# Performance work log

Hardware: AMD Instinct MI355X
Metric: run time of the kernel (lower is better)

The kernel has to match this reference:

```python
import jax, jax.numpy as jnp
import numpy as np

DIM = 512
HEADS = 8
DIM_HEAD = 64
HIDDEN = HEADS * DIM_HEAD  # 512


def setup_inputs() -> dict:
    key = jax.random.key(0)
    k1, k2, k3, k4 = jax.random.split(key, 4)
    x = jax.random.normal(k1, (8, DIM, 64, 64), dtype=jnp.float32)
    # 1x1 conv weights stored as [out_ch, in_ch] (kernel spatial dims are 1)
    w_qkv = jax.random.normal(k2, (HIDDEN * 3, DIM), dtype=jnp.float32) * (1.0 / np.sqrt(DIM))
    w_out = jax.random.normal(k3, (DIM, HIDDEN), dtype=jnp.float32) * (1.0 / np.sqrt(HIDDEN))
    b_out = jax.random.normal(k4, (DIM,), dtype=jnp.float32) * 0.01
    return {"x": x, "w_qkv": w_qkv, "w_out": w_out, "b_out": b_out}


def reference(x, w_qkv, w_out, b_out):
    b, c, h, w = x.shape
    n = h * w
    # to_qkv: 1x1 conv == per-pixel GEMM over channels
    qkv = jnp.einsum('bchw,oc->bohw', x, w_qkv)            # [b, 3*hidden, h, w]
    qkv = qkv.reshape(b, 3, HEADS, DIM_HEAD, n)            # matches torch reshape order
    q, k, v = qkv[:, 0], qkv[:, 1], qkv[:, 2]              # each [b, heads, dim_head, n]
    k = jax.nn.softmax(k, axis=-1)                          # softmax over spatial positions
    context = jnp.einsum('bhdn,bhen->bhde', k, v)          # [b, heads, d, e] kv outer-product
    out = jnp.einsum('bhde,bhdn->bhen', context, q)        # query readout [b, heads, e, n]
    out = out.reshape(b, HEADS * DIM_HEAD, h, w)
    # to_out: 1x1 conv with bias
    return jnp.einsum('bchw,oc->bohw', out, w_out) + b_out[None, :, None, None]
```

## Files before the change

### kernel.cpp

```cpp
#include <hip/hip_runtime.h>
#include <hip/hip_bf16.h>
#include <math.h>

#define NB    8
#define CDIM  512
#define NSP   4096
#define NHEAD 8

typedef short short8 __attribute__((ext_vector_type(8)));
typedef float f32x4  __attribute__((ext_vector_type(4)));

__device__ __forceinline__ unsigned short f2bf(float f) {
    unsigned int u = __float_as_uint(f);
    u += 0x7fff + ((u >> 16) & 1);
    return (unsigned short)(u >> 16);
}
__device__ __forceinline__ float bf2f(unsigned short s) {
    return __uint_as_float(((unsigned int)s) << 16);
}
__device__ __forceinline__ void gld_lds16(const void* g, void* s) {
    __builtin_amdgcn_global_load_lds(
        (const __attribute__((address_space(1))) unsigned int*)g,
        (__attribute__((address_space(3))) unsigned int*)s, 16, 0, 0);
}
__device__ __forceinline__ void split8(const float* s, short8& hi, short8& lo) {
    float4 a = *reinterpret_cast<const float4*>(s);
    float4 b = *reinterpret_cast<const float4*>(s + 4);
    float v[8] = {a.x, a.y, a.z, a.w, b.x, b.y, b.z, b.w};
    #pragma unroll
    for (int j = 0; j < 8; ++j) {
        unsigned short hh = f2bf(v[j]);
        hi[j] = (short)hh;
        lo[j] = (short)f2bf(v[j] - bf2f(hh));
    }
}

__global__ __launch_bounds__(256) void convert_x(const float* __restrict__ x,
    unsigned short* __restrict__ xh, unsigned short* __restrict__ xl)
{
    const int cb4 = blockIdx.x;
    const int kt  = blockIdx.y;
    const int b   = blockIdx.z;
    const int tid = threadIdx.x;

    __shared__ float sx[32][65];

    const int r  = tid >> 3;
    const int c8 = (tid & 7) * 8;
    const float* xp = x + ((long)b * CDIM + kt * 32 + r) * NSP + cb4 * 64 + c8;
    float4 v0 = *reinterpret_cast<const float4*>(xp);
    float4 v1 = *reinterpret_cast<const float4*>(xp + 4);
    sx[r][c8 + 0] = v0.x; sx[r][c8 + 1] = v0.y; sx[r][c8 + 2] = v0.z; sx[r][c8 + 3] = v0.w;
    sx[r][c8 + 4] = v1.x; sx[r][c8 + 5] = v1.y; sx[r][c8 + 6] = v1.z; sx[r][c8 + 7] = v1.w;
    __syncthreads();

    const int cb_l  = tid >> 6;
    const int lane  = tid & 63;
    const int cb    = cb4 * 4 + cb_l;
    const int col_l = cb_l * 16 + (lane & 15);
    const int k0    = (lane >> 4) * 8;
    short8 hv, lv;
    #pragma unroll
    for (int j = 0; j < 8; ++j) {
        float v = sx[k0 + j][col_l];
        unsigned short hh = f2bf(v);
        hv[j] = (short)hh;
        lv[j] = (short)f2bf(v - bf2f(hh));
    }
    const long base = (((long)(b * 256 + cb) * 16 + kt) * 512) + lane * 8;
    *reinterpret_cast<short8*>(xh + base) = hv;
    *reinterpret_cast<short8*>(xl + base) = lv;
}

__global__ __launch_bounds__(64) void convert_w(const float* __restrict__ w,
    unsigned short* __restrict__ wh, unsigned short* __restrict__ wl)
{
    const int lane = threadIdx.x & 63;
    const int rb = blockIdx.x;
    const int kt = blockIdx.y;
    const int row = rb * 16 + (lane & 15);
    const int k0  = kt * 32 + (lane >> 4) * 8;
    const float* wp = w + (long)row * CDIM + k0;
    const long base = ((long)rb * 16 + kt) * 512 + lane * 8;
    short8 hv, lv;
    #pragma unroll
    for (int j = 0; j < 8; ++j) {
        float v = wp[j];
        unsigned short h = f2bf(v);
        hv[j] = (short)h;
        lv[j] = (short)f2bf(v - bf2f(h));
    }
    *reinterpret_cast<short8*>(wh + base) = hv;
    *reinterpret_cast<short8*>(wl + base) = lv;
}

__global__ __launch_bounds__(64) void convert_b(const float* __restrict__ src,
    int ld, unsigned short* __restrict__ bh, unsigned short* __restrict__ bl)
{
    const int lane = threadIdx.x & 63;
    const int cb = blockIdx.x;
    const int kt = blockIdx.y;
    const int col = cb * 16 + (lane & 15);
    const int k0  = kt * 32 + (lane >> 4) * 8;
    const float* sp = src + (long)k0 * ld + col;
    const long base = ((long)cb * 16 + kt) * 512 + lane * 8;
    short8 hv, lv;
    #pragma unroll
    for (int j = 0; j < 8; ++j) {
        float v = sp[(long)j * ld];
        unsigned short h = f2bf(v);
        hv[j] = (short)h;
        lv[j] = (short)f2bf(v - bf2f(h));
    }
    *reinterpret_cast<short8*>(bh + base) = hv;
    *reinterpret_cast<short8*>(bl + base) = lv;
}

__global__ __launch_bounds__(256, 2) void fused_kv_ctx(
    const unsigned short* __restrict__ Ah, const unsigned short* __restrict__ Al,
    const unsigned short* __restrict__ Bh, const unsigned short* __restrict__ Bl,
    float* __restrict__ ctx, float* __restrict__ ssum)
{
    const int ch = blockIdx.x;
    const int h  = blockIdx.y;
    const int b  = blockIdx.z;
    const int tid  = threadIdx.x;
    const int lane = tid & 63;
    const int wid  = tid >> 6;
    const int wr = wid >> 1, wc = wid & 1;

    __shared__ __align__(16) char lds[49152];

    f32x4 acc[4][8];
    #pragma unroll
    for (int m = 0; m < 4; ++m)
        #pragma unroll
        for (int n = 0; n < 8; ++n)
            acc[m][n] = (f32x4){0.f, 0.f, 0.f, 0.f};

    const unsigned short* srcs[12];
    #pragma unroll
    for (int i = 0; i < 12; ++i) {
        const int blk = wid * 12 + i;
        const unsigned short* s;
        if (blk < 16) {
            const int sub = blk & 7;
            const int rb = (sub < 4) ? (h * 4 + sub) : (32 + h * 4 + (sub - 4));
            s = ((blk < 8) ? Ah : Al) + ((long)(rb * 16) << 9);
        } else {
            const int j = (blk - 16) & 15;
            const int cb = ch * 16 + j;
            s = ((blk < 32) ? Bh : Bl) + (((long)(b * 256 + cb) * 16) << 9);
        }
        srcs[i] = s + lane * 8;
    }

    for (int kt = 0; kt < 16; ++kt) {
        #pragma unroll
        for (int i = 0; i < 12; ++i) {
            gld_lds16(srcs[i], lds + (wid * 12 + i) * 1024);
            srcs[i] += 512;
        }
        __syncthreads();

        short8 ah[4], al[4];
        #pragma unroll
        for (int m = 0; m < 4; ++m) {
            ah[m] = *reinterpret_cast<const short8*>(lds +        (wr * 4 + m) * 1024 + lane * 16);
            al[m] = *reinterpret_cast<const short8*>(lds + 8192 + (wr * 4 + m) * 1024 + lane * 16);
        }
        #pragma unroll
        for (int n = 0; n < 8; ++n) {
            short8 bh = *reinterpret_cast<const short8*>(lds + 16384 + (wc * 8 + n) * 1024 + lane * 16);
            short8 bl = *reinterpret_cast<const short8*>(lds + 32768 + (wc * 8 + n) * 1024 + lane * 16);
            #pragma unroll
            for (int m = 0; m < 4; ++m) {
                acc[m][n] = __builtin_amdgcn_mfma_f32_16x16x32_bf16(ah[m], bh, acc[m][n], 0, 0, 0);
                acc[m][n] = __builtin_amdgcn_mfma_f32_16x16x32_bf16(ah[m], bl, acc[m][n], 0, 0, 0);
                acc[m][n] = __builtin_amdgcn_mfma_f32_16x16x32_bf16(al[m], bh, acc[m][n], 0, 0, 0);
            }
        }
        __syncthreads();
    }

    if (wr == 0) {
        #pragma unroll
        for (int m = 0; m < 4; ++m)
            #pragma unroll
            for (int j = 0; j < 4; ++j) {
                float s = 0.f;
                #pragma unroll
                for (int n = 0; n < 8; ++n) {
                    float e = __expf(acc[m][n][j]);
                    acc[m][n][j] = e;
                    s += e;
                }
                s += __shfl_xor(s, 1); s += __shfl_xor(s, 2);
                s += __shfl_xor(s, 4); s += __shfl_xor(s, 8);
                if ((lane & 15) == 0)
                    atomicAdd(&ssum[b * 512 + h * 64 + m * 16 + (lane >> 4) * 4 + j], s);
            }
    }

    float* Plds = (float*)lds;
    float* Vlds = (float*)(lds + 64 * 68 * 4);
    f32x4 acc2[2][2];
    #pragma unroll
    for (int mi = 0; mi < 2; ++mi)
        #pragma unroll
        for (int ni = 0; ni < 2; ++ni) acc2[mi][ni] = (f32x4){0.f, 0.f, 0.f, 0.f};

    #pragma unroll
    for (int q = 0; q < 4; ++q) {
        __syncthreads();
        if (wc == (q >> 1)) {
            float* T = (wr == 0) ? Plds : Vlds;
            #pragma unroll
            for (int m = 0; m < 4; ++m)
                #pragma unroll
                for (int nn = 0; nn < 4; ++nn)
                    #pragma unroll
                    for (int j = 0; j < 4; ++j)
                        T[(m * 16 + (lane >> 4) * 4 + j) * 68 + nn * 16 + (lane & 15)]
                            = acc[m][(q & 1) * 4 + nn][j];
        }
        __syncthreads();

        #pragma unroll
        for (int ks = 0; ks < 2; ++ks) {
            const int kcol = ks * 32 + (lane >> 4) * 8;
            short8 pa_h[2], pa_l[2], vb_h[2], vb_l[2];
            #pragma unroll
            for (int mi = 0; mi < 2; ++mi)
                split8(&Plds[((wr * 2 + mi) * 16 + (lane & 15)) * 68 + kcol], pa_h[mi], pa_l[mi]);
            #pragma unroll
            for (int ni = 0; ni < 2; ++ni)
                split8(&Vlds[((wc * 2 + ni) * 16 + (lane & 15)) * 68 + kcol], vb_h[ni], vb_l[ni]);
            #pragma unroll
            for (int mi = 0; mi < 2; ++mi)
                #pragma unroll
                for (int ni = 0; ni < 2; ++ni) {
                    acc2[mi][ni] = __builtin_amdgcn_mfma_f32_16x16x32_bf16(pa_h[mi], vb_h[ni], acc2[mi][ni], 0, 0, 0);
                    acc2[mi][ni] = __builtin_amdgcn_mfma_f32_16x16x32_bf16(pa_h[mi], vb_l[ni], acc2[mi][ni], 0, 0, 0);
                    acc2[mi][ni] = __builtin_amdgcn_mfma_f32_16x16x32_bf16(pa_l[mi], vb_h[ni], acc2[mi][ni], 0, 0, 0);
                }
        }
    }

    float* cp = ctx + (long)(b * NHEAD + h) * 4096;
    #pragma unroll
    for (int mi = 0; mi < 2; ++mi)
        #pragma unroll
        for (int ni = 0; ni < 2; ++ni) {
            const int d0 = (wr * 2 + mi) * 16;
            const int e0 = (wc * 2 + ni) * 16;
            #pragma unroll
            for (int j = 0; j < 4; ++j)
                atomicAdd(&cp[(d0 + (lane >> 4) * 4 + j) * 64 + e0 + (lane & 15)], acc2[mi][ni][j]);
        }
}

template<int NKT, bool BIAS>
__global__ __launch_bounds__(512, 2) void gemm_mfma256(
    const unsigned short* __restrict__ Ah, const unsigned short* __restrict__ Al,
    const unsigned short* __restrict__ Bh, const unsigned short* __restrict__ Bl,
    float* __restrict__ C, const float* __restrict__ bias,
    int N, int aBatchRB, int bBatchCB, long cBatch)
{
    const int b    = blockIdx.z;
    const int tid  = threadIdx.x;
    const int lane = tid & 63;
    const int wid  = tid >> 6;
    const int wr   = wid >> 2;
    const int wc   = wid & 3;

    __shared__ __align__(16) char lds[2][65536];

    f32x4 acc[8][4];
    #pragma unroll
    for (int m = 0; m < 8; ++m)
        #pragma unroll
        for (int n = 0; n < 4; ++n)
            acc[m][n] = (f32x4){0.f, 0.f, 0.f, 0.f};

    const int rb0 = b * aBatchRB + blockIdx.y * 16;
    const int cb0 = b * bBatchCB + blockIdx.x * 16;

    const unsigned short* srcs[8];
    #pragma unroll
    for (int i = 0; i < 8; ++i) {
        const int blk = wid * 8 + i;
        const int sub = blk & 15;
        const unsigned short* s;
        if (blk < 16)      s = Ah + ((long)(rb0 + sub) * NKT << 9);
        else if (blk < 32) s = Al + ((long)(rb0 + sub) * NKT << 9);
        else if (blk < 48) s = Bh + ((long)(cb0 + sub) * NKT << 9);
        else               s = Bl + ((long)(cb0 + sub) * NKT << 9);
        srcs[i] = s + lane * 8;
    }
    const int ldsoff = wid * 8192;

    #pragma unroll
    for (int i = 0; i < 8; ++i) {
        gld_lds16(srcs[i], &lds[0][ldsoff + i * 1024]);
        srcs[i] += 512;
    }

    int cur = 0;
    for (int kt = 0; kt < NKT; ++kt) {
        if (kt + 1 < NKT) {
            #pragma unroll
            for (int i = 0; i < 8; ++i) {
                gld_lds16(srcs[i], &lds[cur ^ 1][ldsoff + i * 1024]);
                srcs[i] += 512;
            }
            asm volatile("s_waitcnt vmcnt(8)" ::: "memory");
        } else {
            asm volatile("s_waitcnt vmcnt(0)" ::: "memory");
        }
        __builtin_amdgcn_s_barrier();

        const char* L = lds[cur];
        short8 ah[8], al[8];
        #pragma unroll
        for (int m = 0; m < 8; ++m) {
            ah[m] = *reinterpret_cast<const short8*>(L +         (wr * 8 + m) * 1024 + lane * 16);
            al[m] = *reinterpret_cast<const short8*>(L + 16384 + (wr * 8 + m) * 1024 + lane * 16);
        }
        __builtin_amdgcn_s_setprio(1);
        #pragma unroll
        for (int n = 0; n < 4; ++n) {
            short8 bh = *reinterpret_cast<const short8*>(L + 32768 + (wc * 4 + n) * 1024 + lane * 16);
            short8 bl = *reinterpret_cast<const short8*>(L + 49152 + (wc * 4 + n) * 1024 + lane * 16);
            #pragma unroll
            for (int m = 0; m < 8; ++m) {
                acc[m][n] = __builtin_amdgcn_mfma_f32_16x16x32_bf16(ah[m], bh, acc[m][n], 0, 0, 0);
                acc[m][n] = __builtin_amdgcn_mfma_f32_16x16x32_bf16(ah[m], bl, acc[m][n], 0, 0, 0);
                acc[m][n] = __builtin_amdgcn_mfma_f32_16x16x32_bf16(al[m], bh, acc[m][n], 0, 0, 0);
            }
        }
        __builtin_amdgcn_s_setprio(0);
        asm volatile("" ::: "memory");
        __builtin_amdgcn_s_barrier();
        asm volatile("" ::: "memory");
        cur ^= 1;
    }

    const int row0 = blockIdx.y * 256 + wr * 128;
    const int col0 = blockIdx.x * 256 + wc * 64;
    float* Cb = C + (long)b * cBatch;
    #pragma unroll
    for (int m = 0; m < 8; ++m)
        #pragma unroll
        for (int n = 0; n < 4; ++n) {
            const int col = col0 + n * 16 + (lane & 15);
            #pragma unroll
            for (int j = 0; j < 4; ++j) {
                const int row = row0 + m * 16 + (lane >> 4) * 4 + j;
                float v = acc[m][n][j];
                if (BIAS) v += bias[row];
                Cb[(long)row * N + col] = v;
            }
        }
}

template<int NKT, bool BIAS>
__global__ __launch_bounds__(256) void gemm_mfma(
    const unsigned short* __restrict__ Ah, const unsigned short* __restrict__ Al,
    const unsigned short* __restrict__ Bh, const unsigned short* __restrict__ Bl,
    float* __restrict__ C, const float* __restrict__ bias,
    int N, int aBatchRB, int bBatchCB, long cBatch)
{
    const int b    = blockIdx.z;
    const int tid  = threadIdx.x;
    const int lane = tid & 63;
    const int wid  = tid >> 6;
    const int wr   = wid >> 1;
    const int wc   = wid & 1;

    __shared__ __align__(16) char lds[32768];

    f32x4 acc[4][4];
    #pragma unroll
    for (int m = 0; m < 4; ++m)
        #pragma unroll
        for (int n = 0; n < 4; ++n) acc[m][n] = (f32x4){0.f, 0.f, 0.f, 0.f};

    const int rb0 = b * aBatchRB + blockIdx.y * 8;
    const int cb0 = b * bBatchCB + blockIdx.x * 8;

    const unsigned short* srcs[8];
    #pragma unroll
    for (int i = 0; i < 8; ++i) {
        const int blk = wid * 8 + i;
        const int sub = blk & 7;
        const unsigned short* s;
        if (blk < 8)       s = Ah + ((long)(rb0 + sub) * NKT << 9);
        else if (blk < 16) s = Al + ((long)(rb0 + sub) * NKT << 9);
        else if (blk < 24) s = Bh + ((long)(cb0 + sub) * NKT << 9);
        else               s = Bl + ((long)(cb0 + sub) * NKT << 9);
        srcs[i] = s + lane * 8;
    }

    for (int kt = 0; kt < NKT; ++kt) {
        #pragma unroll
        for (int i = 0; i < 8; ++i) {
            gld_lds16(srcs[i], lds + (wid * 8 + i) * 1024);
            srcs[i] += 512;
        }
        __syncthreads();

        short8 ah[4], al[4], bh[4], bl[4];
        #pragma unroll
        for (int m = 0; m < 4; ++m) {
            ah[m] = *reinterpret_cast<const short8*>(lds +         (wr * 4 + m) * 1024 + lane * 16);
            al[m] = *reinterpret_cast<const short8*>(lds +  8192 + (wr * 4 + m) * 1024 + lane * 16);
        }
        #pragma unroll
        for (int n = 0; n < 4; ++n) {
            bh[n] = *reinterpret_cast<const short8*>(lds + 16384 + (wc * 4 + n) * 1024 + lane * 16);
            bl[n] = *reinterpret_cast<const short8*>(lds + 24576 + (wc * 4 + n) * 1024 + lane * 16);
        }
        #pragma unroll
        for (int m = 0; m < 4; ++m)
            #pragma unroll
            for (int n = 0; n < 4; ++n) {
                acc[m][n] = __builtin_amdgcn_mfma_f32_16x16x32_bf16(ah[m], bh[n], acc[m][n], 0, 0, 0);
                acc[m][n] = __builtin_amdgcn_mfma_f32_16x16x32_bf16(ah[m], bl[n], acc[m][n], 0, 0, 0);
                acc[m][n] = __builtin_amdgcn_mfma_f32_16x16x32_bf16(al[m], bh[n], acc[m][n], 0, 0, 0);
            }
        __syncthreads();
    }

    const int row0 = blockIdx.y * 128 + wr * 64;
    const int col0 = blockIdx.x * 128 + wc * 64;
    float* Cb = C + (long)b * cBatch;
    #pragma unroll
    for (int m = 0; m < 4; ++m)
        #pragma unroll
        for (int n = 0; n < 4; ++n) {
            const int col = col0 + n * 16 + (lane & 15);
            #pragma unroll
            for (int j = 0; j < 4; ++j) {
                const int row = row0 + m * 16 + (lane >> 4) * 4 + j;
                float v = acc[m][n][j];
                if (BIAS) v += bias[row];
                Cb[(long)row * N + col] = v;
            }
        }
}

__global__ __launch_bounds__(256) void zero_buf(float* p, int n) {
    for (int i = blockIdx.x * 256 + threadIdx.x; i < n; i += gridDim.x * 256) p[i] = 0.f;
}

__global__ __launch_bounds__(256) void ctx_fold2(
    const float* __restrict__ w_out, const float* __restrict__ ctx,
    const float* __restrict__ ssum,
    unsigned short* __restrict__ amh, unsigned short* __restrict__ aml)
{
    const int o0 = blockIdx.x * 64;
    const int h  = blockIdx.y;
    const int b  = blockIdx.z;
    const int tid = threadIdx.x;

    __shared__ float Wo[64][65];
    __shared__ float Ct[64][65];
    __shared__ float At[64][65];

    for (int idx = tid; idx < 64 * 16; idx += 256) {
        const int r = idx >> 4;
        const int c = (idx & 15) * 4;
        float4 w4 = *reinterpret_cast<const float4*>(&w_out[(long)(o0 + r) * CDIM + h * 64 + c]);
        Wo[r][c + 0] = w4.x; Wo[r][c + 1] = w4.y; Wo[r][c + 2] = w4.z; Wo[r][c + 3] = w4.w;
        float4 c4 = *reinterpret_cast<const float4*>(&ctx[(((long)(b * NHEAD + h) * 64 + r) * 64) + c]);
        Ct[r][c + 0] = c4.x; Ct[r][c + 1] = c4.y; Ct[r][c + 2] = c4.z; Ct[r][c + 3] = c4.w;
    }
    __syncthreads();

    const int to = tid >> 4, td = tid & 15;
    float acc[4][4];
    #pragma unroll
    for (int i = 0; i < 4; ++i)
        #pragma unroll
        for (int j = 0; j < 4; ++j) acc[i][j] = 0.f;

    for (int e = 0; e < 64; ++e) {
        float ro[4], rd[4];
        #pragma unroll
        for (int i = 0; i < 4; ++i) ro[i] = Wo[to * 4 + i][e];
        #pragma unroll
        for (int j = 0; j < 4; ++j) rd[j] = Ct[td * 4 + j][e];
        #pragma unroll
        for (int i = 0; i < 4; ++i)
            #pragma unroll
            for (int j = 0; j < 4; ++j) acc[i][j] += ro[i] * rd[j];
    }

    #pragma unroll
    for (int j = 0; j < 4; ++j) {
        const float s = 1.f / ssum[b * 512 + h * 64 + td * 4 + j];
        #pragma unroll
        for (int i = 0; i < 4; ++i)
            At[to * 4 + i][td * 4 + j] = acc[i][j] * s;
    }
    __syncthreads();

    const int g = tid >> 6, lane = tid & 63;
    #pragma unroll
    for (int kt_l = 0; kt_l < 2; ++kt_l) {
        short8 hv, lv;
        #pragma unroll
        for (int jj = 0; jj < 8; ++jj) {
            float v = At[g * 16 + (lane & 15)][kt_l * 32 + (lane >> 4) * 8 + jj];
            unsigned short hh = f2bf(v);
            hv[jj] = (short)hh;
            lv[jj] = (short)f2bf(v - bf2f(hh));
        }
        const long base = (((long)(b * 32 + (o0 >> 4) + g) * 16) + (h * 2 + kt_l)) * 512 + lane * 8;
        *reinterpret_cast<short8*>(amh + base) = hv;
        *reinterpret_cast<short8*>(aml + base) = lv;
    }
}

extern "C" void kernel_launch(void* const* d_in, const int* in_sizes, int n_in,
                              void* d_out, int out_size, void* d_ws, size_t ws_size,
                              hipStream_t stream) {
    (void)in_sizes; (void)n_in; (void)out_size; (void)ws_size;
    const float* x     = (const float*)d_in[0];
    const float* w_qkv = (const float*)d_in[1];
    const float* w_out = (const float*)d_in[2];
    const float* b_out = (const float*)d_in[3];
    float* out = (float*)d_out;

    char* ws = (char*)d_ws;
    unsigned short* xh   = (unsigned short*)(ws + 134217728L);
    unsigned short* xl   = (unsigned short*)(ws + 167772160L);
    unsigned short* wkvh = (unsigned short*)(ws + 201326592L);
    unsigned short* wkvl = (unsigned short*)(ws + 202375168L);
    float*          ssum = (float*)(ws + 203423744L);
    float*          ctx  = (float*)(ws + 203440128L);
    float*          W3   = (float*)(ws + 8388608L);
    unsigned short* amh  = (unsigned short*)(ws + 16777216L);
    unsigned short* aml  = (unsigned short*)(ws + 20971520L);
    unsigned short* wqh  = (unsigned short*)(ws + 25165824L);
    unsigned short* wql  = (unsigned short*)(ws + 26214400L);
    unsigned short* w3h  = (unsigned short*)(ws + 27262976L);
    unsigned short* w3l  = (unsigned short*)(ws + 31457280L);

    convert_x<<<dim3(64, 16, NB), 256, 0, stream>>>(x, xh, xl);
    convert_w<<<dim3(64, 16), 64, 0, stream>>>(w_qkv + 512L * CDIM, wkvh, wkvl);
    zero_buf<<<256, 256, 0, stream>>>(ssum, (16384 + 1048576) / 4);

    fused_kv_ctx<<<dim3(16, NHEAD, NB), 256, 0, stream>>>(
        wkvh, wkvl, xh, xl, ctx, ssum);

    convert_b<<<dim3(32, 16), 64, 0, stream>>>(w_qkv, CDIM, wqh, wql);

    ctx_fold2<<<dim3(8, NHEAD, NB), 256, 0, stream>>>(w_out, ctx, ssum, amh, aml);

    gemm_mfma<16, false><<<dim3(4, 4, NB), 256, 0, stream>>>(
        amh, aml, wqh, wql, W3, nullptr, CDIM, 32, 0, (long)CDIM * CDIM);

    convert_w<<<dim3(256, 16), 64, 0, stream>>>(W3, w3h, w3l);
    gemm_mfma256<16, true><<<dim3(16, 2, NB), 512, 0, stream>>>(
        w3h, w3l, xh, xl, out, b_out, NSP, 32, 256, (long)CDIM * NSP);
}
```

Measured before the change: 219.1 us.

## Widen fused_kv_ctx to 512 threads and fuse W3 GEMM with bf16 split conversion

The fused K/V context kernel now runs 8 waves per block instead of 4. Each wave handles half as many column tiles, which cuts accumulator registers and allows more waves to be resident. Separately, the W3 GEMM epilogue now stages its results through LDS and writes the bf16 hi/lo split tiles directly. This removes the fp32 W3 round trip through global memory and one kernel launch. The cost is extra LDS staging and more barriers in the epilogue.

```diff
diff --git a/kernel.cpp b/kernel.cpp
--- a/kernel.cpp
+++ b/kernel.cpp
@@ -116,7 +116,7 @@
     *reinterpret_cast<short8*>(bl + base) = lv;
 }
 
-__global__ __launch_bounds__(256, 2) void fused_kv_ctx(
+__global__ __launch_bounds__(512, 4) void fused_kv_ctx(
     const unsigned short* __restrict__ Ah, const unsigned short* __restrict__ Al,
     const unsigned short* __restrict__ Bh, const unsigned short* __restrict__ Bl,
     float* __restrict__ ctx, float* __restrict__ ssum)
@@ -127,21 +127,22 @@
     const int tid  = threadIdx.x;
     const int lane = tid & 63;
     const int wid  = tid >> 6;
-    const int wr = wid >> 1, wc = wid & 1;
+    const int wr = wid >> 2;
+    const int wc = wid & 3;
 
     __shared__ __align__(16) char lds[49152];
 
-    f32x4 acc[4][8];
+    f32x4 acc[4][4];
     #pragma unroll
     for (int m = 0; m < 4; ++m)
         #pragma unroll
-        for (int n = 0; n < 8; ++n)
+        for (int n = 0; n < 4; ++n)
             acc[m][n] = (f32x4){0.f, 0.f, 0.f, 0.f};
 
-    const unsigned short* srcs[12];
-    #pragma unroll
-    for (int i = 0; i < 12; ++i) {
-        const int blk = wid * 12 + i;
+    const unsigned short* srcs[6];
+    #pragma unroll
+    for (int i = 0; i < 6; ++i) {
+        const int blk = wid * 6 + i;
         const unsigned short* s;
         if (blk < 16) {
             const int sub = blk & 7;
@@ -157,8 +158,8 @@
 
     for (int kt = 0; kt < 16; ++kt) {
         #pragma unroll
-        for (int i = 0; i < 12; ++i) {
-            gld_lds16(srcs[i], lds + (wid * 12 + i) * 1024);
+        for (int i = 0; i < 6; ++i) {
+            gld_lds16(srcs[i], lds + (wid * 6 + i) * 1024);
             srcs[i] += 512;
         }
         __syncthreads();
@@ -170,9 +171,9 @@
             al[m] = *reinterpret_cast<const short8*>(lds + 8192 + (wr * 4 + m) * 1024 + lane * 16);
         }
         #pragma unroll
-        for (int n = 0; n < 8; ++n) {
-            short8 bh = *reinterpret_cast<const short8*>(lds + 16384 + (wc * 8 + n) * 1024 + lane * 16);
-            short8 bl = *reinterpret_cast<const short8*>(lds + 32768 + (wc * 8 + n) * 1024 + lane * 16);
+        for (int n = 0; n < 4; ++n) {
+            short8 bh = *reinterpret_cast<const short8*>(lds + 16384 + (wc * 4 + n) * 1024 + lane * 16);
+            short8 bl = *reinterpret_cast<const short8*>(lds + 32768 + (wc * 4 + n) * 1024 + lane * 16);
             #pragma unroll
             for (int m = 0; m < 4; ++m) {
                 acc[m][n] = __builtin_amdgcn_mfma_f32_16x16x32_bf16(ah[m], bh, acc[m][n], 0, 0, 0);
@@ -190,7 +191,7 @@
             for (int j = 0; j < 4; ++j) {
                 float s = 0.f;
                 #pragma unroll
-                for (int n = 0; n < 8; ++n) {
+                for (int n = 0; n < 4; ++n) {
                     float e = __expf(acc[m][n][j]);
                     acc[m][n][j] = e;
                     s += e;
@@ -204,60 +205,52 @@
 
     float* Plds = (float*)lds;
     float* Vlds = (float*)(lds + 64 * 68 * 4);
-    f32x4 acc2[2][2];
-    #pragma unroll
-    for (int mi = 0; mi < 2; ++mi)
-        #pragma unroll
-        for (int ni = 0; ni < 2; ++ni) acc2[mi][ni] = (f32x4){0.f, 0.f, 0.f, 0.f};
+    f32x4 acc2[2];
+    acc2[0] = (f32x4){0.f, 0.f, 0.f, 0.f};
+    acc2[1] = (f32x4){0.f, 0.f, 0.f, 0.f};
 
     #pragma unroll
     for (int q = 0; q < 4; ++q) {
         __syncthreads();
-        if (wc == (q >> 1)) {
+        if (wc == q) {
             float* T = (wr == 0) ? Plds : Vlds;
             #pragma unroll
             for (int m = 0; m < 4; ++m)
                 #pragma unroll
-                for (int nn = 0; nn < 4; ++nn)
+                for (int n = 0; n < 4; ++n)
                     #pragma unroll
                     for (int j = 0; j < 4; ++j)
-                        T[(m * 16 + (lane >> 4) * 4 + j) * 68 + nn * 16 + (lane & 15)]
-                            = acc[m][(q & 1) * 4 + nn][j];
+                        T[(m * 16 + (lane >> 4) * 4 + j) * 68 + n * 16 + (lane & 15)]
+                            = acc[m][n][j];
         }
         __syncthreads();
 
         #pragma unroll
         for (int ks = 0; ks < 2; ++ks) {
             const int kcol = ks * 32 + (lane >> 4) * 8;
-            short8 pa_h[2], pa_l[2], vb_h[2], vb_l[2];
+            short8 pa_h[2], pa_l[2], vb_h, vb_l;
             #pragma unroll
             for (int mi = 0; mi < 2; ++mi)
-                split8(&Plds[((wr * 2 + mi) * 16 + (lane & 15)) * 68 + kcol], pa_h[mi], pa_l[mi]);
-            #pragma unroll
-            for (int ni = 0; ni < 2; ++ni)
-                split8(&Vlds[((wc * 2 + ni) * 16 + (lane & 15)) * 68 + kcol], vb_h[ni], vb_l[ni]);
-            #pragma unroll
-            for (int mi = 0; mi < 2; ++mi)
-                #pragma unroll
-                for (int ni = 0; ni < 2; ++ni) {
-                    acc2[mi][ni] = __builtin_amdgcn_mfma_f32_16x16x32_bf16(pa_h[mi], vb_h[ni], acc2[mi][ni], 0, 0, 0);
-                    acc2[mi][ni] = __builtin_amdgcn_mfma_f32_16x16x32_bf16(pa_h[mi], vb_l[ni], acc2[mi][ni], 0, 0, 0);
-                    acc2[mi][ni] = __builtin_amdgcn_mfma_f32_16x16x32_bf16(pa_l[mi], vb_h[ni], acc2[mi][ni], 0, 0, 0);
-                }
+                split8(&Plds[(wr * 32 + mi * 16 + (lane & 15)) * 68 + kcol], pa_h[mi], pa_l[mi]);
+            split8(&Vlds[(wc * 16 + (lane & 15)) * 68 + kcol], vb_h, vb_l);
+            #pragma unroll
+            for (int mi = 0; mi < 2; ++mi) {
+                acc2[mi] = __builtin_amdgcn_mfma_f32_16x16x32_bf16(pa_h[mi], vb_h, acc2[mi], 0, 0, 0);
+                acc2[mi] = __builtin_amdgcn_mfma_f32_16x16x32_bf16(pa_h[mi], vb_l, acc2[mi], 0, 0, 0);
+                acc2[mi] = __builtin_amdgcn_mfma_f32_16x16x32_bf16(pa_l[mi], vb_h, acc2[mi], 0, 0, 0);
+            }
         }
     }
 
     float* cp = ctx + (long)(b * NHEAD + h) * 4096;
     #pragma unroll
-    for (int mi = 0; mi < 2; ++mi)
-        #pragma unroll
-        for (int ni = 0; ni < 2; ++ni) {
-            const int d0 = (wr * 2 + mi) * 16;
-            const int e0 = (wc * 2 + ni) * 16;
-            #pragma unroll
-            for (int j = 0; j < 4; ++j)
-                atomicAdd(&cp[(d0 + (lane >> 4) * 4 + j) * 64 + e0 + (lane & 15)], acc2[mi][ni][j]);
-        }
+    for (int mi = 0; mi < 2; ++mi) {
+        const int d0 = wr * 32 + mi * 16;
+        const int e  = wc * 16 + (lane & 15);
+        #pragma unroll
+        for (int j = 0; j < 4; ++j)
+            atomicAdd(&cp[(d0 + (lane >> 4) * 4 + j) * 64 + e], acc2[mi][j]);
+    }
 }
 
 template<int NKT, bool BIAS>
@@ -364,12 +357,14 @@
         }
 }
 
-template<int NKT, bool BIAS>
-__global__ __launch_bounds__(256) void gemm_mfma(
+__global__ __launch_bounds__(256) void zero_buf(float* p, int n) {
+    for (int i = blockIdx.x * 256 + threadIdx.x; i < n; i += gridDim.x * 256) p[i] = 0.f;
+}
+
+__global__ __launch_bounds__(256) void gemm_w3(
     const unsigned short* __restrict__ Ah, const unsigned short* __restrict__ Al,
     const unsigned short* __restrict__ Bh, const unsigned short* __restrict__ Bl,
-    float* __restrict__ C, const float* __restrict__ bias,
-    int N, int aBatchRB, int bBatchCB, long cBatch)
+    unsigned short* __restrict__ w3h, unsigned short* __restrict__ w3l)
 {
     const int b    = blockIdx.z;
     const int tid  = threadIdx.x;
@@ -378,7 +373,7 @@
     const int wr   = wid >> 1;
     const int wc   = wid & 1;
 
-    __shared__ __align__(16) char lds[32768];
+    __shared__ __align__(16) char lds[64 * 132 * 4];
 
     f32x4 acc[4][4];
     #pragma unroll
@@ -386,8 +381,8 @@
         #pragma unroll
         for (int n = 0; n < 4; ++n) acc[m][n] = (f32x4){0.f, 0.f, 0.f, 0.f};
 
-    const int rb0 = b * aBatchRB + blockIdx.y * 8;
-    const int cb0 = b * bBatchCB + blockIdx.x * 8;
+    const int rb0 = b * 32 + blockIdx.y * 8;
+    const int cb0 = blockIdx.x * 8;
 
     const unsigned short* srcs[8];
     #pragma unroll
@@ -395,14 +390,14 @@
         const int blk = wid * 8 + i;
         const int sub = blk & 7;
         const unsigned short* s;
-        if (blk < 8)       s = Ah + ((long)(rb0 + sub) * NKT << 9);
-        else if (blk < 16) s = Al + ((long)(rb0 + sub) * NKT << 9);
-        else if (blk < 24) s = Bh + ((long)(cb0 + sub) * NKT << 9);
-        else               s = Bl + ((long)(cb0 + sub) * NKT << 9);
+        if (blk < 8)       s = Ah + ((long)(rb0 + sub) * 16 << 9);
+        else if (blk < 16) s = Al + ((long)(rb0 + sub) * 16 << 9);
+        else if (blk < 24) s = Bh + ((long)(cb0 + sub) * 16 << 9);
+        else               s = Bl + ((long)(cb0 + sub) * 16 << 9);
         srcs[i] = s + lane * 8;
     }
 
-    for (int kt = 0; kt < NKT; ++kt) {
+    for (int kt = 0; kt < 16; ++kt) {
         #pragma unroll
         for (int i = 0; i < 8; ++i) {
             gld_lds16(srcs[i], lds + (wid * 8 + i) * 1024);
@@ -432,26 +427,40 @@
         __syncthreads();
     }
 
-    const int row0 = blockIdx.y * 128 + wr * 64;
-    const int col0 = blockIdx.x * 128 + wc * 64;
-    float* Cb = C + (long)b * cBatch;
-    #pragma unroll
-    for (int m = 0; m < 4; ++m)
-        #pragma unroll
-        for (int n = 0; n < 4; ++n) {
-            const int col = col0 + n * 16 + (lane & 15);
-            #pragma unroll
-            for (int j = 0; j < 4; ++j) {
-                const int row = row0 + m * 16 + (lane >> 4) * 4 + j;
-                float v = acc[m][n][j];
-                if (BIAS) v += bias[row];
-                Cb[(long)row * N + col] = v;
-            }
-        }
-}
-
-__global__ __launch_bounds__(256) void zero_buf(float* p, int n) {
-    for (int i = blockIdx.x * 256 + threadIdx.x; i < n; i += gridDim.x * 256) p[i] = 0.f;
+    float* Ct = (float*)lds;
+    #pragma unroll
+    for (int hf = 0; hf < 2; ++hf) {
+        __syncthreads();
+        if (wr == hf) {
+            #pragma unroll
+            for (int m = 0; m < 4; ++m)
+                #pragma unroll
+                for (int n = 0; n < 4; ++n)
+                    #pragma unroll
+                    for (int j = 0; j < 4; ++j)
+                        Ct[(m * 16 + (lane >> 4) * 4 + j) * 132 + wc * 64 + n * 16 + (lane & 15)]
+                            = acc[m][n][j];
+        }
+        __syncthreads();
+        #pragma unroll
+        for (int i = 0; i < 4; ++i) {
+            const int blkid = wid * 4 + i;
+            const int rbl = blkid >> 2, ktl = blkid & 3;
+            short8 hv, lv;
+            #pragma unroll
+            for (int jj = 0; jj < 8; ++jj) {
+                float v = Ct[(rbl * 16 + (lane & 15)) * 132 + ktl * 32 + (lane >> 4) * 8 + jj];
+                unsigned short hh = f2bf(v);
+                hv[jj] = (short)hh;
+                lv[jj] = (short)f2bf(v - bf2f(hh));
+            }
+            const int rbG = b * 32 + blockIdx.y * 8 + hf * 4 + rbl;
+            const int ktG = blockIdx.x * 4 + ktl;
+            const long base = ((long)rbG * 16 + ktG) * 512 + lane * 8;
+            *reinterpret_cast<short8*>(w3h + base) = hv;
+            *reinterpret_cast<short8*>(w3l + base) = lv;
+        }
+    }
 }
 
 __global__ __launch_bounds__(256) void ctx_fold2(
@@ -540,7 +549,6 @@
     unsigned short* wkvl = (unsigned short*)(ws + 202375168L);
     float*          ssum = (float*)(ws + 203423744L);
     float*          ctx  = (float*)(ws + 203440128L);
-    float*          W3   = (float*)(ws + 8388608L);
     unsigned short* amh  = (unsigned short*)(ws + 16777216L);
     unsigned short* aml  = (unsigned short*)(ws + 20971520L);
     unsigned short* wqh  = (unsigned short*)(ws + 25165824L);
@@ -552,17 +560,15 @@
     convert_w<<<dim3(64, 16), 64, 0, stream>>>(w_qkv + 512L * CDIM, wkvh, wkvl);
     zero_buf<<<256, 256, 0, stream>>>(ssum, (16384 + 1048576) / 4);
 
-    fused_kv_ctx<<<dim3(16, NHEAD, NB), 256, 0, stream>>>(
+    fused_kv_ctx<<<dim3(16, NHEAD, NB), 512, 0, stream>>>(
         wkvh, wkvl, xh, xl, ctx, ssum);
 
     convert_b<<<dim3(32, 16), 64, 0, stream>>>(w_qkv, CDIM, wqh, wql);
 
     ctx_fold2<<<dim3(8, NHEAD, NB), 256, 0, stream>>>(w_out, ctx, ssum, amh, aml);
 
-    gemm_mfma<16, false><<<dim3(4, 4, NB), 256, 0, stream>>>(
-        amh, aml, wqh, wql, W3, nullptr, CDIM, 32, 0, (long)CDIM * CDIM);
-
-    convert_w<<<dim3(256, 16), 64, 0, stream>>>(W3, w3h, w3l);
+    gemm_w3<<<dim3(4, 4, NB), 256, 0, stream>>>(amh, aml, wqh, wql, w3h, w3l);
+
     gemm_mfma256<16, true><<<dim3(16, 2, NB), 512, 0, stream>>>(
         w3h, w3l, xh, xl, out, b_out, NSP, 32, 256, (long)CDIM * NSP);
 }
```

After: 235.1 us. 1.07x slower.
